# Kernel tuning notes

Hardware: AMD Instinct MI355X
Metric: run time of the kernel (lower is better)

## Reference

```python
import jax, jax.numpy as jnp
import numpy as np

EPS = 1e-9


def setup_inputs() -> dict:
    key = jax.random.key(0)
    kx, kw = jax.random.split(key)
    B, S, D, E = 4, 4096, 4096, 64
    x = jax.random.normal(kx, (B, S, D), dtype=jnp.float32)
    # nn.Linear(d_model, num_experts, bias=False): weight shape (E, D)
    W_gate = jax.random.normal(kw, (E, D), dtype=jnp.float32) * (1.0 / np.sqrt(D))
    return {"x": x, "W_gate": W_gate}


def reference(x, W_gate):
    # logits: (B, S, E) = x @ W_gate^T
    logits = jnp.einsum("bsd,ed->bse", x, W_gate)
    probs = jax.nn.softmax(logits, axis=-1)
    top_k = 2
    weights, indices = jax.lax.top_k(probs, top_k)  # (B, S, K) each
    weights = weights / (jnp.sum(weights, axis=-1, keepdims=True) + EPS)
    return indices, weights, logits
```

## Files before the change

### kernel.cpp

```cpp
#include <hip/hip_runtime.h>
#include <math.h>

#define TOKENS 16384
#define DD 4096
#define NE 64
#define MBLK 256
#define KB 32
#define XPITCH 33

__global__ __launch_bounds__(256, 2)
void k1_gemm(const float* __restrict__ x, const float* __restrict__ Wg,
             float* __restrict__ part, int S, int kPerSlice) {
  __shared__ float xs[MBLK * XPITCH];
  __shared__ float wt[KB * NE];

  const int nm   = TOKENS / MBLK;
  const int mblk = blockIdx.x % nm;
  const int s    = blockIdx.x / nm;
  const int tid  = threadIdx.x;
  const int lane = tid & 63;
  const int wid  = tid >> 6;
  const int e0   = wid * 16;
  const long t0  = (long)mblk * MBLK;
  const int k0   = s * kPerSlice;
  const int nchunk = kPerSlice / KB;

  const int xrow = tid >> 3;
  const int xcol = (tid & 7) << 2;
  const int wrow = tid >> 2;
  const int wcol = (tid & 3) << 3;

  const float* xbase = x + t0 * DD + k0;
  const float* wbase = Wg + (long)wrow * DD + k0 + wcol;

  float4 xr[8]; float4 wr0, wr1;
#pragma unroll
  for (int j = 0; j < 8; ++j)
    xr[j] = *(const float4*)(xbase + (long)(xrow + 32 * j) * DD + xcol);
  wr0 = *(const float4*)(wbase);
  wr1 = *(const float4*)(wbase + 4);

  float acc[4][16];
#pragma unroll
  for (int j = 0; j < 4; ++j)
#pragma unroll
    for (int q = 0; q < 16; ++q) acc[j][q] = 0.f;

  const int xb0 = lane * XPITCH;
  const int xb1 = (lane + 64) * XPITCH;
  const int xb2 = (lane + 128) * XPITCH;
  const int xb3 = (lane + 192) * XPITCH;

  for (int c = 0; c < nchunk; ++c) {
#pragma unroll
    for (int j = 0; j < 8; ++j) {
      float* p = &xs[(xrow + 32 * j) * XPITCH + xcol];
      p[0] = xr[j].x; p[1] = xr[j].y; p[2] = xr[j].z; p[3] = xr[j].w;
    }
    {
      const float* w0 = &wr0.x; const float* w1 = &wr1.x;
#pragma unroll
      for (int i = 0; i < 4; ++i) wt[(wcol + i) * NE + wrow] = w0[i];
#pragma unroll
      for (int i = 0; i < 4; ++i) wt[(wcol + 4 + i) * NE + wrow] = w1[i];
    }
    __syncthreads();
    if (c + 1 < nchunk) {
      const float* xb = xbase + (c + 1) * KB;
#pragma unroll
      for (int j = 0; j < 8; ++j)
        xr[j] = *(const float4*)(xb + (long)(xrow + 32 * j) * DD + xcol);
      wr0 = *(const float4*)(wbase + (c + 1) * KB);
      wr1 = *(const float4*)(wbase + (c + 1) * KB + 4);
    }
#pragma unroll 8
    for (int kk = 0; kk < KB; ++kk) {
      float xv0 = xs[xb0 + kk], xv1 = xs[xb1 + kk];
      float xv2 = xs[xb2 + kk], xv3 = xs[xb3 + kk];
      const float4* wv = (const float4*)&wt[kk * NE + e0];
#pragma unroll
      for (int q = 0; q < 4; ++q) {
        float4 wq = wv[q];
        acc[0][4*q+0] += xv0 * wq.x; acc[0][4*q+1] += xv0 * wq.y;
        acc[0][4*q+2] += xv0 * wq.z; acc[0][4*q+3] += xv0 * wq.w;
        acc[1][4*q+0] += xv1 * wq.x; acc[1][4*q+1] += xv1 * wq.y;
        acc[1][4*q+2] += xv1 * wq.z; acc[1][4*q+3] += xv1 * wq.w;
        acc[2][4*q+0] += xv2 * wq.x; acc[2][4*q+1] += xv2 * wq.y;
        acc[2][4*q+2] += xv2 * wq.z; acc[2][4*q+3] += xv2 * wq.w;
        acc[3][4*q+0] += xv3 * wq.x; acc[3][4*q+1] += xv3 * wq.y;
        acc[3][4*q+2] += xv3 * wq.z; acc[3][4*q+3] += xv3 * wq.w;
      }
    }
    __syncthreads();
  }

  float* pb = part + (long)s * TOKENS * NE + (t0 + lane) * NE + e0;
#pragma unroll
  for (int j = 0; j < 4; ++j) {
    float* pr = pb + (long)j * 64 * NE;
#pragma unroll
    for (int q = 0; q < 4; ++q)
      *(float4*)(pr + 4 * q) =
          make_float4(acc[j][4*q], acc[j][4*q+1], acc[j][4*q+2], acc[j][4*q+3]);
  }
}

__global__ __launch_bounds__(256)
void k2_finish(const float* __restrict__ part, int S, float* __restrict__ out) {
  const int tid  = threadIdx.x;
  const int lane = tid & 63;
  const int wv   = tid >> 6;
  const long t   = (long)blockIdx.x * 4 + wv;

  const float* p = part + t * NE + lane;
  float logit = 0.f;
  for (int s = 0; s < S; ++s) logit += p[(long)s * TOKENS * NE];

  out[4 * TOKENS + t * NE + lane] = logit;

  float v = logit; int i = lane;
#pragma unroll
  for (int off = 32; off; off >>= 1) {
    float ov = __shfl_xor(v, off);
    int   oi = __shfl_xor(i, off);
    if (ov > v || (ov == v && oi < i)) { v = ov; i = oi; }
  }
  const float m = v; const int i1 = i;

  float v2 = (lane == i1) ? -INFINITY : logit;
  float vv = v2; int ii = lane;
#pragma unroll
  for (int off = 32; off; off >>= 1) {
    float ov = __shfl_xor(vv, off);
    int   oi = __shfl_xor(ii, off);
    if (ov > vv || (ov == vv && oi < ii)) { vv = ov; ii = oi; }
  }
  const int i2 = ii;

  float z = expf(logit - m);
  float Z = z;
#pragma unroll
  for (int off = 32; off; off >>= 1) Z += __shfl_xor(Z, off);

  float p1 = __shfl(z, i1) / Z;
  float p2 = __shfl(z, i2) / Z;

  if (lane == 0) {
    float denom = p1 + p2 + 1e-9f;
    out[t * 2 + 0] = (float)i1;
    out[t * 2 + 1] = (float)i2;
    out[2 * TOKENS + t * 2 + 0] = p1 / denom;
    out[2 * TOKENS + t * 2 + 1] = p2 / denom;
  }
}

extern "C" void kernel_launch(void* const* d_in, const int* in_sizes, int n_in,
                              void* d_out, int out_size, void* d_ws, size_t ws_size,
                              hipStream_t stream) {
  const float* x  = (const float*)d_in[0];
  const float* Wg = (const float*)d_in[1];
  float* out = (float*)d_out;

  const size_t sliceBytes = (size_t)TOKENS * NE * sizeof(float);
  int S = 8;
  while (S > 1 && (size_t)S * sliceBytes > ws_size) S >>= 1;
  float* part;
  if ((size_t)S * sliceBytes <= ws_size) {
    part = (float*)d_ws;
  } else {
    S = 1;
    part = out + 4 * TOKENS;
  }
  const int kPerSlice = DD / S;

  k1_gemm<<<dim3((TOKENS / MBLK) * S), 256, 0, stream>>>(x, Wg, part, S, kPerSlice);
  k2_finish<<<dim3(TOKENS / 4), 256, 0, stream>>>(part, S, out);
}
```

Before: 406.5 us.

## Replace LDS-tiled gate GEMM with per-thread token rows and pre-transposed weights

Adds a small kernel that transposes W_gate into a k-major workspace buffer. The GEMM kernel drops shared-memory tiling and barriers: each thread now owns one token, keeps all 64 expert accumulators in registers, and streams its own x row from global memory with simple register prefetch. The weight row for each k is the same address across the wavefront, so it can be served by uniform or scalar loads. The aim is to remove LDS traffic and synchronisation, at the cost of strided, uncoalesced x reads across lanes and higher register pressure.

```diff
diff --git a/kernel.cpp b/kernel.cpp
--- a/kernel.cpp
+++ b/kernel.cpp
@@ -5,104 +5,61 @@
 #define DD 4096
 #define NE 64
 #define MBLK 256
-#define KB 32
-#define XPITCH 33
+
+__global__ void k0_transpose(const float* __restrict__ Wg, float* __restrict__ WT) {
+  const int k0 = blockIdx.x * 64;
+  const int e  = threadIdx.x & 63;
+  const int kq = threadIdx.x >> 6;
+#pragma unroll
+  for (int kk = 0; kk < 16; ++kk) {
+    const int k = k0 + kq * 16 + kk;
+    WT[(long)k * NE + e] = Wg[(long)e * DD + k];
+  }
+}
 
 __global__ __launch_bounds__(256, 2)
-void k1_gemm(const float* __restrict__ x, const float* __restrict__ Wg,
-             float* __restrict__ part, int S, int kPerSlice) {
-  __shared__ float xs[MBLK * XPITCH];
-  __shared__ float wt[KB * NE];
-
+void k1_gemm(const float* __restrict__ x, const float* __restrict__ WT,
+             float* __restrict__ part, int kPerSlice) {
   const int nm   = TOKENS / MBLK;
   const int mblk = blockIdx.x % nm;
   const int s    = blockIdx.x / nm;
   const int tid  = threadIdx.x;
-  const int lane = tid & 63;
-  const int wid  = tid >> 6;
-  const int e0   = wid * 16;
-  const long t0  = (long)mblk * MBLK;
+  const long t   = (long)mblk * MBLK + tid;
   const int k0   = s * kPerSlice;
-  const int nchunk = kPerSlice / KB;
 
-  const int xrow = tid >> 3;
-  const int xcol = (tid & 7) << 2;
-  const int wrow = tid >> 2;
-  const int wcol = (tid & 3) << 3;
+  const float* xp = x + t * (long)DD + k0;
+  const float* wk = WT + (long)k0 * NE;
 
-  const float* xbase = x + t0 * DD + k0;
-  const float* wbase = Wg + (long)wrow * DD + k0 + wcol;
+  float acc[NE];
+#pragma unroll
+  for (int e = 0; e < NE; ++e) acc[e] = 0.f;
 
-  float4 xr[8]; float4 wr0, wr1;
+  float4 a = *(const float4*)(xp);
+  float4 b = *(const float4*)(xp + 4);
+
+  for (int kb = 0; kb < kPerSlice; kb += 8) {
+    float4 an, bn;
+    const bool more = (kb + 8 < kPerSlice);
+    if (more) {
+      an = *(const float4*)(xp + kb + 8);
+      bn = *(const float4*)(xp + kb + 12);
+    }
+    const float* w8 = wk + (long)kb * NE;
 #pragma unroll
-  for (int j = 0; j < 8; ++j)
-    xr[j] = *(const float4*)(xbase + (long)(xrow + 32 * j) * DD + xcol);
-  wr0 = *(const float4*)(wbase);
-  wr1 = *(const float4*)(wbase + 4);
-
-  float acc[4][16];
+    for (int kq = 0; kq < 8; ++kq) {
+      const float xvk = (kq < 4) ? (&a.x)[kq] : (&b.x)[kq - 4];
+      const float* wrow = w8 + kq * NE;
 #pragma unroll
-  for (int j = 0; j < 4; ++j)
-#pragma unroll
-    for (int q = 0; q < 16; ++q) acc[j][q] = 0.f;
-
-  const int xb0 = lane * XPITCH;
-  const int xb1 = (lane + 64) * XPITCH;
-  const int xb2 = (lane + 128) * XPITCH;
-  const int xb3 = (lane + 192) * XPITCH;
-
-  for (int c = 0; c < nchunk; ++c) {
-#pragma unroll
-    for (int j = 0; j < 8; ++j) {
-      float* p = &xs[(xrow + 32 * j) * XPITCH + xcol];
-      p[0] = xr[j].x; p[1] = xr[j].y; p[2] = xr[j].z; p[3] = xr[j].w;
+      for (int e = 0; e < NE; ++e) acc[e] += wrow[e] * xvk;
     }
-    {
-      const float* w0 = &wr0.x; const float* w1 = &wr1.x;
-#pragma unroll
-      for (int i = 0; i < 4; ++i) wt[(wcol + i) * NE + wrow] = w0[i];
-#pragma unroll
-      for (int i = 0; i < 4; ++i) wt[(wcol + 4 + i) * NE + wrow] = w1[i];
-    }
-    __syncthreads();
-    if (c + 1 < nchunk) {
-      const float* xb = xbase + (c + 1) * KB;
-#pragma unroll
-      for (int j = 0; j < 8; ++j)
-        xr[j] = *(const float4*)(xb + (long)(xrow + 32 * j) * DD + xcol);
-      wr0 = *(const float4*)(wbase + (c + 1) * KB);
-      wr1 = *(const float4*)(wbase + (c + 1) * KB + 4);
-    }
-#pragma unroll 8
-    for (int kk = 0; kk < KB; ++kk) {
-      float xv0 = xs[xb0 + kk], xv1 = xs[xb1 + kk];
-      float xv2 = xs[xb2 + kk], xv3 = xs[xb3 + kk];
-      const float4* wv = (const float4*)&wt[kk * NE + e0];
-#pragma unroll
-      for (int q = 0; q < 4; ++q) {
-        float4 wq = wv[q];
-        acc[0][4*q+0] += xv0 * wq.x; acc[0][4*q+1] += xv0 * wq.y;
-        acc[0][4*q+2] += xv0 * wq.z; acc[0][4*q+3] += xv0 * wq.w;
-        acc[1][4*q+0] += xv1 * wq.x; acc[1][4*q+1] += xv1 * wq.y;
-        acc[1][4*q+2] += xv1 * wq.z; acc[1][4*q+3] += xv1 * wq.w;
-        acc[2][4*q+0] += xv2 * wq.x; acc[2][4*q+1] += xv2 * wq.y;
-        acc[2][4*q+2] += xv2 * wq.z; acc[2][4*q+3] += xv2 * wq.w;
-        acc[3][4*q+0] += xv3 * wq.x; acc[3][4*q+1] += xv3 * wq.y;
-        acc[3][4*q+2] += xv3 * wq.z; acc[3][4*q+3] += xv3 * wq.w;
-      }
-    }
-    __syncthreads();
+    if (more) { a = an; b = bn; }
   }
 
-  float* pb = part + (long)s * TOKENS * NE + (t0 + lane) * NE + e0;
+  float* pb = part + ((long)s * TOKENS + t) * NE;
 #pragma unroll
-  for (int j = 0; j < 4; ++j) {
-    float* pr = pb + (long)j * 64 * NE;
-#pragma unroll
-    for (int q = 0; q < 4; ++q)
-      *(float4*)(pr + 4 * q) =
-          make_float4(acc[j][4*q], acc[j][4*q+1], acc[j][4*q+2], acc[j][4*q+3]);
-  }
+  for (int q = 0; q < 16; ++q)
+    *(float4*)(pb + 4 * q) =
+        make_float4(acc[4*q], acc[4*q+1], acc[4*q+2], acc[4*q+3]);
 }
 
 __global__ __launch_bounds__(256)
@@ -127,8 +84,7 @@
   }
   const float m = v; const int i1 = i;
 
-  float v2 = (lane == i1) ? -INFINITY : logit;
-  float vv = v2; int ii = lane;
+  float vv = (lane == i1) ? -INFINITY : logit; int ii = lane;
 #pragma unroll
   for (int off = 32; off; off >>= 1) {
     float ov = __shfl_xor(vv, off);
@@ -161,18 +117,20 @@
   const float* Wg = (const float*)d_in[1];
   float* out = (float*)d_out;
 
+  float* WT = (float*)d_ws;
+  const size_t wtBytes    = (size_t)DD * NE * sizeof(float);
   const size_t sliceBytes = (size_t)TOKENS * NE * sizeof(float);
+
   int S = 8;
-  while (S > 1 && (size_t)S * sliceBytes > ws_size) S >>= 1;
-  float* part;
-  if ((size_t)S * sliceBytes <= ws_size) {
-    part = (float*)d_ws;
-  } else {
+  while (S > 1 && wtBytes + (size_t)S * sliceBytes > ws_size) S >>= 1;
+  float* part = (float*)((char*)d_ws + wtBytes);
+  if (wtBytes + sliceBytes > ws_size) {
     S = 1;
     part = out + 4 * TOKENS;
   }
   const int kPerSlice = DD / S;
 
-  k1_gemm<<<dim3((TOKENS / MBLK) * S), 256, 0, stream>>>(x, Wg, part, S, kPerSlice);
+  k0_transpose<<<dim3(DD / 64), 256, 0, stream>>>(Wg, WT);
+  k1_gemm<<<dim3((TOKENS / MBLK) * S), 256, 0, stream>>>(x, WT, part, kPerSlice);
   k2_finish<<<dim3(TOKENS / 4), 256, 0, stream>>>(part, S, out);
 }
```

New measurement: 514.9 us. 1.27x slower.
